# Optimization experiments

Measured on AMD Instinct MI355X. Metric: run time of the kernel, lower is better.

Reference implementation:

```python
import jax, jax.numpy as jnp
import numpy as np

EPS = 1e-6      # zero-token detection eps
LN_EPS = 1e-5   # torch LayerNorm default
H = 8           # num_heads


def setup_inputs() -> dict:
    key = jax.random.key(0)
    ks = jax.random.split(key, 6)
    B, T, D = 4, 2048, 512
    embs = jax.random.normal(ks[0], (B, T, D), jnp.float32)
    labels = jax.random.uniform(ks[1], (B, T), jnp.float32)
    s = 1.0 / np.sqrt(D)
    ln_g = jnp.ones((D,), jnp.float32)
    ln_b = jnp.zeros((D,), jnp.float32)
    in_proj_w = jax.random.uniform(ks[2], (3 * D, D), jnp.float32, -s, s)
    in_proj_b = jnp.zeros((3 * D,), jnp.float32)
    out_w = jax.random.uniform(ks[3], (D, D), jnp.float32, -s, s)
    out_b = jnp.zeros((D,), jnp.float32)
    alpha = jnp.float32(1.0)
    beta = jnp.float32(0.0)
    return {"embs": embs, "labels": labels, "ln_g": ln_g, "ln_b": ln_b,
            "in_proj_w": in_proj_w, "in_proj_b": in_proj_b,
            "out_w": out_w, "out_b": out_b, "alpha": alpha, "beta": beta}


def reference(embs, labels, ln_g, ln_b, in_proj_w, in_proj_b, out_w, out_b, alpha, beta):
    B, T, D = embs.shape
    h, dh = H, D // H
    # pre-LayerNorm
    mu = embs.mean(-1, keepdims=True)
    var = ((embs - mu) ** 2).mean(-1, keepdims=True)
    x = (embs - mu) / jnp.sqrt(var + LN_EPS) * ln_g + ln_b
    # key padding mask from all-zero tokens (computed on normalized x, as in source)
    kpm = jnp.abs(x).sum(-1) <= EPS                      # [B,T] bool
    w = jnp.where(kpm, jnp.float32(0.0), labels)         # zero labels on masked tokens
    # fused qkv projection (nn.MultiheadAttention in_proj)
    qkv = x @ in_proj_w.T + in_proj_b                    # [B,T,3D]
    q, k, v = jnp.split(qkv, 3, axis=-1)
    def sp(a):
        return a.reshape(B, T, h, dh).transpose(0, 2, 1, 3)  # [B,h,T,dh]
    q, k, v = sp(q), sp(k), sp(v)
    scores = jnp.einsum('bhqd,bhkd->bhqk', q, k) / np.sqrt(dh)
    # additive label bias: alpha * labels (broadcast over heads & queries) + beta
    scores = scores + (alpha * w[:, None, None, :] + beta)
    # key padding mask -> -inf (use large negative for stability)
    scores = jnp.where(kpm[:, None, None, :], jnp.float32(-1e30), scores)
    a = jax.nn.softmax(scores, axis=-1)
    o = jnp.einsum('bhqk,bhkd->bhqd', a, v).transpose(0, 2, 1, 3).reshape(B, T, D)
    o = o @ out_w.T + out_b
    o = jnp.nan_to_num(o, nan=0.0, posinf=0.0, neginf=0.0)
    # masked mean pool over T
    m = (~kpm)[..., None].astype(o.dtype)                # [B,T,1]
    pooled = (o * m).sum(1) / jnp.maximum(m.sum(1), 1.0)  # [B,D]
    return pooled
```

## Files before the change

kernel.cpp:

```cpp
#include <hip/hip_runtime.h>
#include <math.h>

#define T 2048
#define D 512
#define NH 8
#define DH 64
#define NB 4
#define NTOK (NB * T)
#define LOG2E 1.44269504f
#define QSCALE (0.125f * LOG2E)

using bf16x8 = __attribute__((ext_vector_type(8))) short;
using f32x4  = __attribute__((ext_vector_type(4))) float;

static __device__ __forceinline__ unsigned short f2bf(float f) {
    union { float f; unsigned u; } v; v.f = f;
    unsigned r = v.u + 0x7fffu + ((v.u >> 16) & 1u);
    return (unsigned short)(r >> 16);
}
#if __has_builtin(__builtin_amdgcn_cvt_pk_bf16_f32)
static __device__ __forceinline__ unsigned pack_bf16_pair(float a, float b) {
    auto r = __builtin_amdgcn_cvt_pk_bf16_f32(a, b);
    union { decltype(r) v; unsigned u; } c; c.v = r;
    return c.u;
}
#else
static __device__ __forceinline__ unsigned pack_bf16_pair(float a, float b) {
    union { float f; unsigned u; } ua, ub; ua.f = a; ub.f = b;
    unsigned ra = ua.u + 0x7fffu + ((ua.u >> 16) & 1u);
    unsigned rb = ub.u + 0x7fffu + ((ub.u >> 16) & 1u);
    return __builtin_amdgcn_perm(rb, ra, 0x07060302);
}
#endif


__global__ __launch_bounds__(256) void ln_kernel(
    const float* __restrict__ embs, const float* __restrict__ labels,
    const float* __restrict__ g, const float* __restrict__ bb,
    const float* __restrict__ alpha_p, const float* __restrict__ beta_p,
    unsigned short* __restrict__ xfrag, float* __restrict__ wexp,
    float* __restrict__ kpmf)
{
    __shared__ __align__(16) unsigned short Xs[16][520];
    int tid = threadIdx.x, wave = tid >> 6, lane = tid & 63;
    int quad = lane >> 4, lm = lane & 15;
    int t16 = blockIdx.x;

    float4 g0 = *(const float4*)(g + lane * 8), g1 = *(const float4*)(g + lane * 8 + 4);
    float4 c0 = *(const float4*)(bb + lane * 8), c1 = *(const float4*)(bb + lane * 8 + 4);
    float gv[8] = {g0.x, g0.y, g0.z, g0.w, g1.x, g1.y, g1.z, g1.w};
    float cv[8] = {c0.x, c0.y, c0.z, c0.w, c1.x, c1.y, c1.z, c1.w};

    for (int tt = 0; tt < 4; ++tt) {
        int n = t16 * 16 + wave * 4 + tt;
        const float* e = embs + (size_t)n * D + lane * 8;
        float4 a4 = *(const float4*)e, b4 = *(const float4*)(e + 4);
        float v[8] = {a4.x, a4.y, a4.z, a4.w, b4.x, b4.y, b4.z, b4.w};

        float s = 0.f, ss = 0.f;
        #pragma unroll
        for (int j = 0; j < 8; ++j) { s += v[j]; ss += v[j] * v[j]; }
        #pragma unroll
        for (int o = 1; o <= 32; o <<= 1) {
            s += __shfl_xor(s, o, 64);
            ss += __shfl_xor(ss, o, 64);
        }
        float mu = s * (1.0f / D);
        float var = ss * (1.0f / D) - mu * mu;
        float rstd = rsqrtf(var + 1e-5f);

        float x[8], as = 0.f;
        #pragma unroll
        for (int j = 0; j < 8; ++j) {
            x[j] = (v[j] - mu) * rstd * gv[j] + cv[j];
            as += fabsf(x[j]);
        }
        uint4 pk;
        pk.x = pack_bf16_pair(x[0], x[1]);
        pk.y = pack_bf16_pair(x[2], x[3]);
        pk.z = pack_bf16_pair(x[4], x[5]);
        pk.w = pack_bf16_pair(x[6], x[7]);
        *(uint4*)&Xs[wave * 4 + tt][lane * 8] = pk;

        #pragma unroll
        for (int o = 1; o <= 32; o <<= 1) as += __shfl_xor(as, o, 64);
        if (lane == 0) {
            int kpm = (as <= 1e-6f);
            kpmf[n] = kpm ? 1.0f : 0.0f;
            wexp[n] = kpm ? 0.0f : __expf(alpha_p[0] * labels[n] + beta_p[0]);
        }
    }
    __syncthreads();
    #pragma unroll
    for (int i = 0; i < 4; ++i) {
        int kc = wave * 4 + i;
        bf16x8 fr = *(const bf16x8*)&Xs[lm][kc * 32 + quad * 8];
        *(bf16x8*)(xfrag + ((size_t)(t16 * 16 + kc) * 64 + lane) * 8) = fr;
    }
}

__global__ __launch_bounds__(256) void wconv_kernel(
    const float* __restrict__ w, unsigned short* __restrict__ wbfrag)
{
    __shared__ __align__(16) unsigned short Ws[16][520];
    int tid = threadIdx.x, wave = tid >> 6, lane = tid & 63;
    int quad = lane >> 4, lm = lane & 15;
    int j16 = blockIdx.x;

    for (int tt = 0; tt < 4; ++tt) {
        int j = j16 * 16 + wave * 4 + tt;
        const float* wp = w + (size_t)j * D + lane * 8;
        float4 a4 = *(const float4*)wp, b4 = *(const float4*)(wp + 4);
        uint4 pk;
        pk.x = pack_bf16_pair(a4.x, a4.y);
        pk.y = pack_bf16_pair(a4.z, a4.w);
        pk.z = pack_bf16_pair(b4.x, b4.y);
        pk.w = pack_bf16_pair(b4.z, b4.w);
        *(uint4*)&Ws[wave * 4 + tt][lane * 8] = pk;
    }
    __syncthreads();
    #pragma unroll
    for (int i = 0; i < 4; ++i) {
        int kc = wave * 4 + i;
        bf16x8 fr = *(const bf16x8*)&Ws[lm][kc * 32 + quad * 8];
        *(bf16x8*)(wbfrag + ((size_t)(j16 * 16 + kc) * 64 + lane) * 8) = fr;
    }
}

__global__ __launch_bounds__(256) void wfrag_fill(
    const float* __restrict__ wexp, unsigned short* __restrict__ vfrag)
{
    int idx = blockIdx.x * 256 + threadIdx.x;
    int lane = idx & 63, chunk = idx >> 6;
    int kk = chunk & 1, t64 = (chunk >> 1) & 31, bh = chunk >> 6;
    int lm = lane & 15, quad = lane >> 4;
    int b_ = bh >> 3;
    size_t base = (((size_t)chunk * 5 + 4) * 64 + lane) * 8;
    if (lm == 0) {
        int key0 = t64 * 64 + kk * 32 + quad * 8;
        const float* wp = wexp + b_ * T + key0;
        unsigned short vv[8];
        #pragma unroll
        for (int e = 0; e < 8; ++e) vv[e] = f2bf(wp[e]);
        *(uint4*)(vfrag + base) = *(uint4*)vv;
    } else {
        uint4 z = {0u, 0u, 0u, 0u};
        *(uint4*)(vfrag + base) = z;
    }
}

__global__ __launch_bounds__(256) void qkv_mfma(
    const unsigned short* __restrict__ xfrag, const unsigned short* __restrict__ wbfrag,
    const float* __restrict__ bias, const float* __restrict__ wexp,
    unsigned short* __restrict__ qfrag, unsigned short* __restrict__ kfrag,
    unsigned short* __restrict__ vfrag)
{
    __shared__ __align__(16) unsigned short Ls[4][64][72];
    int tid = threadIdx.x;
    int wave = tid >> 6, lane = tid & 63, quad = lane >> 4, lm = lane & 15;
    int wr = wave >> 1, wc = wave & 1;
    int m0 = blockIdx.x * 128 + wr * 64;
    int j0 = blockIdx.y * 128 + wc * 64;
    int mt16 = m0 >> 4, jt16 = j0 >> 4;

    f32x4 acc[4][4];
    #pragma unroll
    for (int a = 0; a < 4; ++a)
        #pragma unroll
        for (int b = 0; b < 4; ++b) acc[a][b] = (f32x4){0.f,0.f,0.f,0.f};

    bf16x8 af0[4], bf0[4], af1[4], bf1[4];
    auto load_ab = [&](int kc, bf16x8 (&af)[4], bf16x8 (&bf)[4]) {
        #pragma unroll
        for (int mf = 0; mf < 4; ++mf)
            af[mf] = *(const bf16x8*)(xfrag + ((size_t)((mt16 + mf) * 16 + kc) * 64 + lane) * 8);
        #pragma unroll
        for (int nt = 0; nt < 4; ++nt)
            bf[nt] = *(const bf16x8*)(wbfrag + ((size_t)((jt16 + nt) * 16 + kc) * 64 + lane) * 8);
    };
    auto do_mfma = [&](bf16x8 (&af)[4], bf16x8 (&bf)[4]) {
        #pragma unroll
        for (int mf = 0; mf < 4; ++mf)
            #pragma unroll
            for (int nt = 0; nt < 4; ++nt)
                acc[mf][nt] = __builtin_amdgcn_mfma_f32_16x16x32_bf16(af[mf], bf[nt], acc[mf][nt], 0, 0, 0);
    };

    load_ab(0, af0, bf0);
    for (int kc = 0; kc < 16; kc += 2) {
        load_ab(kc + 1, af1, bf1);
        do_mfma(af0, bf0);
        load_ab((kc + 2) & 15, af0, bf0);
        do_mfma(af1, bf1);
    }

    int part = j0 >> 9;
    int h = (j0 & 511) >> 6;
    int b_ = m0 >> 11, tloc = m0 & (T - 1);
    int bh = b_ * NH + h;
    float bcol[4];
    #pragma unroll
    for (int nt = 0; nt < 4; ++nt) bcol[nt] = bias[j0 + nt * 16 + lm];

    if (part == 2) {
        float wv[4][4];
        #pragma unroll
        for (int mf = 0; mf < 4; ++mf)
            #pragma unroll
            for (int r = 0; r < 4; ++r)
                wv[mf][r] = wexp[b_ * T + tloc + mf * 16 + quad * 4 + r];
        #pragma unroll
        for (int mf = 0; mf < 4; ++mf)
            #pragma unroll
            for (int nt = 0; nt < 4; ++nt) {
                uint2 pw;
                pw.x = pack_bf16_pair((acc[mf][nt][0] + bcol[nt]) * wv[mf][0],
                                      (acc[mf][nt][1] + bcol[nt]) * wv[mf][1]);
                pw.y = pack_bf16_pair((acc[mf][nt][2] + bcol[nt]) * wv[mf][2],
                                      (acc[mf][nt][3] + bcol[nt]) * wv[mf][3]);
                *(uint2*)&Ls[wave][nt * 16 + lm][mf * 16 + quad * 4] = pw;
            }
        #pragma unroll
        for (int nt = 0; nt < 4; ++nt)
            #pragma unroll
            for (int kk = 0; kk < 2; ++kk) {
                bf16x8 fr = *(const bf16x8*)&Ls[wave][nt * 16 + lm][kk * 32 + quad * 8];
                size_t chunk = ((((size_t)bh * 32 + (tloc >> 6)) * 2 + kk) * 5) + nt;
                *(bf16x8*)(vfrag + chunk * 512 + lane * 8) = fr;
            }
    } else {
        float scale = (part == 0) ? QSCALE : 1.0f;
        #pragma unroll
        for (int mf = 0; mf < 4; ++mf)
            #pragma unroll
            for (int nt = 0; nt < 4; ++nt)
                #pragma unroll
                for (int r = 0; r < 4; ++r)
                    Ls[wave][mf * 16 + quad * 4 + r][nt * 16 + lm] =
                        f2bf((acc[mf][nt][r] + bcol[nt]) * scale);
        if (part == 0) {
            #pragma unroll
            for (int mf = 0; mf < 4; ++mf)
                #pragma unroll
                for (int kk = 0; kk < 2; ++kk) {
                    bf16x8 fr = *(const bf16x8*)&Ls[wave][mf * 16 + lm][kk * 32 + quad * 8];
                    size_t chunk = ((size_t)bh * 128 + (tloc >> 4) + mf) * 2 + kk;
                    *(bf16x8*)(qfrag + chunk * 512 + lane * 8) = fr;
                }
        } else {
            #pragma unroll
            for (int nta = 0; nta < 4; ++nta)
                #pragma unroll
                for (int kk = 0; kk < 2; ++kk) {
                    bf16x8 fr = *(const bf16x8*)&Ls[wave][lm * 4 + nta][kk * 32 + quad * 8];
                    size_t chunk = ((((size_t)bh * 32 + (tloc >> 6)) * 2 + kk) * 4) + nta;
                    *(bf16x8*)(kfrag + chunk * 512 + lane * 8) = fr;
                }
        }
    }
}

__global__ __launch_bounds__(256, 2) void attn_mfma(
    const unsigned short* __restrict__ qfrag, const unsigned short* __restrict__ kfrag,
    const unsigned short* __restrict__ vfrag, const float* __restrict__ kpmf,
    float* __restrict__ S)
{
    __shared__ __align__(16) unsigned short Ps[4][64][72];
    __shared__ float Lx[2][2][64];
    int g = blockIdx.x;
    int bh = g & 31, q0 = (g >> 5) * 128;
    int tid = threadIdx.x, wave = tid >> 6, lane = tid & 63;
    int quad = lane >> 4, lm = lane & 15;
    int qh = wave >> 1, ks = wave & 1;
    int qbase = q0 + qh * 64;
    int b_ = bh >> 3, h = bh & 7;

    bf16x8 qf[4][2];
    int t16b = (qbase >> 4);
    #pragma unroll
    for (int mf = 0; mf < 4; ++mf)
        #pragma unroll
        for (int kk = 0; kk < 2; ++kk)
            qf[mf][kk] = *(const bf16x8*)(qfrag +
                (((size_t)(bh * 128 + t16b + mf) * 2 + kk) * 64 + lane) * 8);

    f32x4 accO[4][4], accL[4];
    #pragma unroll
    for (int mf = 0; mf < 4; ++mf) {
        #pragma unroll
        for (int nt = 0; nt < 4; ++nt) accO[mf][nt] = (f32x4){0.f,0.f,0.f,0.f};
        accL[mf] = (f32x4){0.f,0.f,0.f,0.f};
    }

    const unsigned short* kb = kfrag + (size_t)bh * 32 * 8 * 512 + (size_t)lane * 8;
    const unsigned short* vb = vfrag + (size_t)bh * 32 * 10 * 512 + (size_t)lane * 8;
    int t0k = ks * 16;

    bf16x8 kf0[4][2], kf1[4][2];
    auto load_k = [&](int t64, bf16x8 (&kf)[4][2]) {
        const unsigned short* p = kb + (size_t)t64 * 8 * 512;
        #pragma unroll
        for (int kk = 0; kk < 2; ++kk)
            #pragma unroll
            for (int nt = 0; nt < 4; ++nt)
                kf[nt][kk] = *(const bf16x8*)(p + ((size_t)kk * 4 + nt) * 512);
    };

    auto process = [&](int t64, bf16x8 (&kf)[4][2]) {
        const unsigned short* p = vb + (size_t)t64 * 10 * 512;
        bf16x8 vf[5][2];
        #pragma unroll
        for (int kk = 0; kk < 2; ++kk)
            #pragma unroll
            for (int nt = 0; nt < 5; ++nt)
                vf[nt][kk] = *(const bf16x8*)(p + ((size_t)kk * 5 + nt) * 512);

        #pragma unroll
        for (int mf = 0; mf < 4; ++mf) {
            f32x4 s[4];
            #pragma unroll
            for (int nt = 0; nt < 4; ++nt) {
                f32x4 t0 = (f32x4){0.f,0.f,0.f,0.f};
                t0 = __builtin_amdgcn_mfma_f32_16x16x32_bf16(qf[mf][0], kf[nt][0], t0, 0, 0, 0);
                t0 = __builtin_amdgcn_mfma_f32_16x16x32_bf16(qf[mf][1], kf[nt][1], t0, 0, 0, 0);
                s[nt] = t0;
            }
            int rowb = mf * 16 + quad * 4;
            #pragma unroll
            for (int r = 0; r < 4; ++r) {
                float p0 = __builtin_amdgcn_exp2f(s[0][r]);
                float p1 = __builtin_amdgcn_exp2f(s[1][r]);
                float p2 = __builtin_amdgcn_exp2f(s[2][r]);
                float p3 = __builtin_amdgcn_exp2f(s[3][r]);
                uint2 pw;
                pw.x = pack_bf16_pair(p0, p1);
                pw.y = pack_bf16_pair(p2, p3);
                *(uint2*)&Ps[wave][rowb + r][lm * 4] = pw;
            }
        }

        bf16x8 pf[4][2];
        #pragma unroll
        for (int mf = 0; mf < 4; ++mf)
            #pragma unroll
            for (int kk = 0; kk < 2; ++kk)
                pf[mf][kk] = *(const bf16x8*)&Ps[wave][mf * 16 + lm][kk * 32 + quad * 8];

        #pragma unroll
        for (int mf = 0; mf < 4; ++mf) {
            #pragma unroll
            for (int nt = 0; nt < 4; ++nt) {
                accO[mf][nt] = __builtin_amdgcn_mfma_f32_16x16x32_bf16(pf[mf][0], vf[nt][0], accO[mf][nt], 0, 0, 0);
                accO[mf][nt] = __builtin_amdgcn_mfma_f32_16x16x32_bf16(pf[mf][1], vf[nt][1], accO[mf][nt], 0, 0, 0);
            }
            accL[mf] = __builtin_amdgcn_mfma_f32_16x16x32_bf16(pf[mf][0], vf[4][0], accL[mf], 0, 0, 0);
            accL[mf] = __builtin_amdgcn_mfma_f32_16x16x32_bf16(pf[mf][1], vf[4][1], accL[mf], 0, 0, 0);
        }
    };

    load_k(t0k, kf0);
    for (int i = 0; i < 16; i += 2) {
        load_k(t0k + i + 1, kf1);
        process(t0k + i, kf0);
        load_k(t0k + ((i + 2) & 15), kf0);
        process(t0k + i + 1, kf1);
    }

    if (lm == 0) {
        #pragma unroll
        for (int mf = 0; mf < 4; ++mf)
            #pragma unroll
            for (int r = 0; r < 4; ++r)
                Lx[qh][ks][mf * 16 + quad * 4 + r] = accL[mf][r];
    }
    __syncthreads();

    float pooled[4] = {0.f, 0.f, 0.f, 0.f};
    #pragma unroll
    for (int mf = 0; mf < 4; ++mf)
        #pragma unroll
        for (int r = 0; r < 4; ++r) {
            int rloc = mf * 16 + quad * 4 + r;
            float l = Lx[qh][0][rloc] + Lx[qh][1][rloc];
            float w = (1.0f - kpmf[b_ * T + qbase + rloc]) / l;
            #pragma unroll
            for (int nt = 0; nt < 4; ++nt) pooled[nt] += accO[mf][nt][r] * w;
        }
    #pragma unroll
    for (int nt = 0; nt < 4; ++nt) {
        pooled[nt] += __shfl_xor(pooled[nt], 16, 64);
        pooled[nt] += __shfl_xor(pooled[nt], 32, 64);
    }
    if (quad == 0) {
        #pragma unroll
        for (int nt = 0; nt < 4; ++nt)
            atomicAdd(&S[b_ * D + h * DH + nt * 16 + lm], pooled[nt]);
    }
}

__global__ __launch_bounds__(256) void out_kernel(
    const float* __restrict__ S, const float* __restrict__ kpmf,
    const float* __restrict__ Wo, const float* __restrict__ bo,
    float* __restrict__ out)
{
    __shared__ float Sl[512];
    __shared__ float cs[4];
    __shared__ float pr[4][64];
    int b_ = blockIdx.x >> 3;
    int cg = blockIdx.x & 7;
    int tid = threadIdx.x;
    int col = tid & 63, kq = tid >> 6;
    Sl[tid] = S[b_ * D + tid];
    Sl[tid + 256] = S[b_ * D + tid + 256];
    const float* kp = kpmf + b_ * T;
    float c = 0.f;
    for (int t = tid; t < T; t += 256) c += kp[t];
    #pragma unroll
    for (int o = 32; o; o >>= 1) c += __shfl_xor(c, o, 64);
    if ((tid & 63) == 0) cs[tid >> 6] = c;
    __syncthreads();
    float masked = cs[0] + cs[1] + cs[2] + cs[3];
    float cnt = (float)T - masked;
    float inv = 1.0f / fmaxf(cnt, 1.0f);

    int d = cg * 64 + col;
    const float4* wr4 = (const float4*)(Wo + (size_t)d * D + kq * 128);
    float dot = 0.f;
    #pragma unroll 8
    for (int i = 0; i < 32; ++i) {
        float4 w4 = wr4[i];
        int kbase = kq * 128 + i * 4;
        dot += Sl[kbase + 0] * w4.x + Sl[kbase + 1] * w4.y +
               Sl[kbase + 2] * w4.z + Sl[kbase + 3] * w4.w;
    }
    pr[kq][col] = dot;
    __syncthreads();
    if (kq == 0) {
        float tot = pr[0][col] + pr[1][col] + pr[2][col] + pr[3][col];
        out[b_ * D + d] = (tot + bo[d] * cnt) * inv;
    }
}

extern "C" void kernel_launch(void* const* d_in, const int* in_sizes, int n_in,
                              void* d_out, int out_size, void* d_ws, size_t ws_size,
                              hipStream_t stream) {
    const float* embs   = (const float*)d_in[0];
    const float* labels = (const float*)d_in[1];
    const float* ln_g   = (const float*)d_in[2];
    const float* ln_b   = (const float*)d_in[3];
    const float* ipw    = (const float*)d_in[4];
    const float* ipb    = (const float*)d_in[5];
    const float* ow     = (const float*)d_in[6];
    const float* obb    = (const float*)d_in[7];
    const float* alpha  = (const float*)d_in[8];
    const float* beta   = (const float*)d_in[9];
    float* out = (float*)d_out;

    unsigned short* xfrag  = (unsigned short*)d_ws;
    unsigned short* wbfrag = xfrag + (size_t)NTOK * D;
    unsigned short* qfrag  = wbfrag + (size_t)3 * D * D;
    unsigned short* kfrag  = qfrag + (size_t)NTOK * D;
    unsigned short* vfrag  = kfrag + (size_t)NTOK * D;
    float* wexp = (float*)(vfrag + (size_t)32 * 32 * 2 * 5 * 512);
    float* kpmf = wexp + NTOK;
    float* S    = kpmf + NTOK;

    hipMemsetAsync(S, 0, (size_t)NB * D * sizeof(float), stream);
    ln_kernel<<<NTOK / 16, 256, 0, stream>>>(embs, labels, ln_g, ln_b, alpha, beta,
                                             xfrag, wexp, kpmf);
    wconv_kernel<<<(3 * D) / 16, 256, 0, stream>>>(ipw, wbfrag);
    wfrag_fill<<<512, 256, 0, stream>>>(wexp, vfrag);
    dim3 gq(NTOK / 128, (3 * D) / 128);
    qkv_mfma<<<gq, 256, 0, stream>>>(xfrag, wbfrag, ipb, wexp, qfrag, kfrag, vfrag);
    attn_mfma<<<32 * (T / 128), 256, 0, stream>>>(qfrag, kfrag, vfrag, kpmf, S);
    out_kernel<<<NB * 8, 256, 0, stream>>>(S, kpmf, ow, obb, out);
}
```

Baseline: 165.7 us.

## Merge prep kernels, fold weight-row fill into QKV, split attention keys four ways

The LayerNorm and weight-conversion kernels become one launch that picks its role by block index. The separate wfrag_fill kernel is removed, and its work (writing the exp-label weight row into the V fragments) moves into the V-epilogue of the QKV GEMM. The attention kernel now uses 512 threads with four key-split waves per query half instead of two, which halves each wave's key loop and adds a four-way partial-sum reduction. The aim is to cut launch overhead and raise attention parallelism, at the cost of more LDS per block and a changed occupancy target.

```diff
diff --git a/kernel.cpp b/kernel.cpp
--- a/kernel.cpp
+++ b/kernel.cpp
@@ -34,118 +34,91 @@
 #endif
 
 
-__global__ __launch_bounds__(256) void ln_kernel(
+__global__ __launch_bounds__(256) void prep_kernel(
     const float* __restrict__ embs, const float* __restrict__ labels,
     const float* __restrict__ g, const float* __restrict__ bb,
     const float* __restrict__ alpha_p, const float* __restrict__ beta_p,
-    unsigned short* __restrict__ xfrag, float* __restrict__ wexp,
-    float* __restrict__ kpmf)
+    const float* __restrict__ w,
+    unsigned short* __restrict__ xfrag, unsigned short* __restrict__ wbfrag,
+    float* __restrict__ wexp, float* __restrict__ kpmf)
 {
     __shared__ __align__(16) unsigned short Xs[16][520];
     int tid = threadIdx.x, wave = tid >> 6, lane = tid & 63;
     int quad = lane >> 4, lm = lane & 15;
-    int t16 = blockIdx.x;
-
-    float4 g0 = *(const float4*)(g + lane * 8), g1 = *(const float4*)(g + lane * 8 + 4);
-    float4 c0 = *(const float4*)(bb + lane * 8), c1 = *(const float4*)(bb + lane * 8 + 4);
-    float gv[8] = {g0.x, g0.y, g0.z, g0.w, g1.x, g1.y, g1.z, g1.w};
-    float cv[8] = {c0.x, c0.y, c0.z, c0.w, c1.x, c1.y, c1.z, c1.w};
-
-    for (int tt = 0; tt < 4; ++tt) {
-        int n = t16 * 16 + wave * 4 + tt;
-        const float* e = embs + (size_t)n * D + lane * 8;
-        float4 a4 = *(const float4*)e, b4 = *(const float4*)(e + 4);
-        float v[8] = {a4.x, a4.y, a4.z, a4.w, b4.x, b4.y, b4.z, b4.w};
-
-        float s = 0.f, ss = 0.f;
-        #pragma unroll
-        for (int j = 0; j < 8; ++j) { s += v[j]; ss += v[j] * v[j]; }
-        #pragma unroll
-        for (int o = 1; o <= 32; o <<= 1) {
-            s += __shfl_xor(s, o, 64);
-            ss += __shfl_xor(ss, o, 64);
-        }
-        float mu = s * (1.0f / D);
-        float var = ss * (1.0f / D) - mu * mu;
-        float rstd = rsqrtf(var + 1e-5f);
-
-        float x[8], as = 0.f;
-        #pragma unroll
-        for (int j = 0; j < 8; ++j) {
-            x[j] = (v[j] - mu) * rstd * gv[j] + cv[j];
-            as += fabsf(x[j]);
-        }
-        uint4 pk;
-        pk.x = pack_bf16_pair(x[0], x[1]);
-        pk.y = pack_bf16_pair(x[2], x[3]);
-        pk.z = pack_bf16_pair(x[4], x[5]);
-        pk.w = pack_bf16_pair(x[6], x[7]);
-        *(uint4*)&Xs[wave * 4 + tt][lane * 8] = pk;
-
-        #pragma unroll
-        for (int o = 1; o <= 32; o <<= 1) as += __shfl_xor(as, o, 64);
-        if (lane == 0) {
-            int kpm = (as <= 1e-6f);
-            kpmf[n] = kpm ? 1.0f : 0.0f;
-            wexp[n] = kpm ? 0.0f : __expf(alpha_p[0] * labels[n] + beta_p[0]);
-        }
-    }
-    __syncthreads();
-    #pragma unroll
-    for (int i = 0; i < 4; ++i) {
-        int kc = wave * 4 + i;
-        bf16x8 fr = *(const bf16x8*)&Xs[lm][kc * 32 + quad * 8];
-        *(bf16x8*)(xfrag + ((size_t)(t16 * 16 + kc) * 64 + lane) * 8) = fr;
-    }
-}
-
-__global__ __launch_bounds__(256) void wconv_kernel(
-    const float* __restrict__ w, unsigned short* __restrict__ wbfrag)
-{
-    __shared__ __align__(16) unsigned short Ws[16][520];
-    int tid = threadIdx.x, wave = tid >> 6, lane = tid & 63;
-    int quad = lane >> 4, lm = lane & 15;
-    int j16 = blockIdx.x;
-
-    for (int tt = 0; tt < 4; ++tt) {
-        int j = j16 * 16 + wave * 4 + tt;
-        const float* wp = w + (size_t)j * D + lane * 8;
-        float4 a4 = *(const float4*)wp, b4 = *(const float4*)(wp + 4);
-        uint4 pk;
-        pk.x = pack_bf16_pair(a4.x, a4.y);
-        pk.y = pack_bf16_pair(a4.z, a4.w);
-        pk.z = pack_bf16_pair(b4.x, b4.y);
-        pk.w = pack_bf16_pair(b4.z, b4.w);
-        *(uint4*)&Ws[wave * 4 + tt][lane * 8] = pk;
-    }
-    __syncthreads();
-    #pragma unroll
-    for (int i = 0; i < 4; ++i) {
-        int kc = wave * 4 + i;
-        bf16x8 fr = *(const bf16x8*)&Ws[lm][kc * 32 + quad * 8];
-        *(bf16x8*)(wbfrag + ((size_t)(j16 * 16 + kc) * 64 + lane) * 8) = fr;
-    }
-}
-
-__global__ __launch_bounds__(256) void wfrag_fill(
-    const float* __restrict__ wexp, unsigned short* __restrict__ vfrag)
-{
-    int idx = blockIdx.x * 256 + threadIdx.x;
-    int lane = idx & 63, chunk = idx >> 6;
-    int kk = chunk & 1, t64 = (chunk >> 1) & 31, bh = chunk >> 6;
-    int lm = lane & 15, quad = lane >> 4;
-    int b_ = bh >> 3;
-    size_t base = (((size_t)chunk * 5 + 4) * 64 + lane) * 8;
-    if (lm == 0) {
-        int key0 = t64 * 64 + kk * 32 + quad * 8;
-        const float* wp = wexp + b_ * T + key0;
-        unsigned short vv[8];
-        #pragma unroll
-        for (int e = 0; e < 8; ++e) vv[e] = f2bf(wp[e]);
-        *(uint4*)(vfrag + base) = *(uint4*)vv;
+
+    if (blockIdx.x < 512) {
+        int t16 = blockIdx.x;
+        float4 g0 = *(const float4*)(g + lane * 8), g1 = *(const float4*)(g + lane * 8 + 4);
+        float4 c0 = *(const float4*)(bb + lane * 8), c1 = *(const float4*)(bb + lane * 8 + 4);
+        float gv[8] = {g0.x, g0.y, g0.z, g0.w, g1.x, g1.y, g1.z, g1.w};
+        float cv[8] = {c0.x, c0.y, c0.z, c0.w, c1.x, c1.y, c1.z, c1.w};
+
+        for (int tt = 0; tt < 4; ++tt) {
+            int n = t16 * 16 + wave * 4 + tt;
+            const float* e = embs + (size_t)n * D + lane * 8;
+            float4 a4 = *(const float4*)e, b4 = *(const float4*)(e + 4);
+            float v[8] = {a4.x, a4.y, a4.z, a4.w, b4.x, b4.y, b4.z, b4.w};
+
+            float s = 0.f, ss = 0.f;
+            #pragma unroll
+            for (int j = 0; j < 8; ++j) { s += v[j]; ss += v[j] * v[j]; }
+            #pragma unroll
+            for (int o = 1; o <= 32; o <<= 1) {
+                s += __shfl_xor(s, o, 64);
+                ss += __shfl_xor(ss, o, 64);
+            }
+            float mu = s * (1.0f / D);
+            float var = ss * (1.0f / D) - mu * mu;
+            float rstd = rsqrtf(var + 1e-5f);
+
+            float x[8], as = 0.f;
+            #pragma unroll
+            for (int j = 0; j < 8; ++j) {
+                x[j] = (v[j] - mu) * rstd * gv[j] + cv[j];
+                as += fabsf(x[j]);
+            }
+            uint4 pk;
+            pk.x = pack_bf16_pair(x[0], x[1]);
+            pk.y = pack_bf16_pair(x[2], x[3]);
+            pk.z = pack_bf16_pair(x[4], x[5]);
+            pk.w = pack_bf16_pair(x[6], x[7]);
+            *(uint4*)&Xs[wave * 4 + tt][lane * 8] = pk;
+
+            #pragma unroll
+            for (int o = 1; o <= 32; o <<= 1) as += __shfl_xor(as, o, 64);
+            if (lane == 0) {
+                int kpm = (as <= 1e-6f);
+                kpmf[n] = kpm ? 1.0f : 0.0f;
+                wexp[n] = kpm ? 0.0f : __expf(alpha_p[0] * labels[n] + beta_p[0]);
+            }
+        }
+        __syncthreads();
+        #pragma unroll
+        for (int i = 0; i < 4; ++i) {
+            int kc = wave * 4 + i;
+            bf16x8 fr = *(const bf16x8*)&Xs[lm][kc * 32 + quad * 8];
+            *(bf16x8*)(xfrag + ((size_t)(t16 * 16 + kc) * 64 + lane) * 8) = fr;
+        }
     } else {
-        uint4 z = {0u, 0u, 0u, 0u};
-        *(uint4*)(vfrag + base) = z;
+        int j16 = blockIdx.x - 512;
+        for (int tt = 0; tt < 4; ++tt) {
+            int j = j16 * 16 + wave * 4 + tt;
+            const float* wp = w + (size_t)j * D + lane * 8;
+            float4 a4 = *(const float4*)wp, b4 = *(const float4*)(wp + 4);
+            uint4 pk;
+            pk.x = pack_bf16_pair(a4.x, a4.y);
+            pk.y = pack_bf16_pair(a4.z, a4.w);
+            pk.z = pack_bf16_pair(b4.x, b4.y);
+            pk.w = pack_bf16_pair(b4.z, b4.w);
+            *(uint4*)&Xs[wave * 4 + tt][lane * 8] = pk;
+        }
+        __syncthreads();
+        #pragma unroll
+        for (int i = 0; i < 4; ++i) {
+            int kc = wave * 4 + i;
+            bf16x8 fr = *(const bf16x8*)&Xs[lm][kc * 32 + quad * 8];
+            *(bf16x8*)(wbfrag + ((size_t)(j16 * 16 + kc) * 64 + lane) * 8) = fr;
+        }
     }
 }
 
@@ -228,6 +201,26 @@
                 size_t chunk = ((((size_t)bh * 32 + (tloc >> 6)) * 2 + kk) * 5) + nt;
                 *(bf16x8*)(vfrag + chunk * 512 + lane * 8) = fr;
             }
+        {
+            int hsel = wave & 1, tsel = wave >> 1;
+            int hbase = ((blockIdx.y * 128) & 511) >> 6;
+            int t64base = ((blockIdx.x * 128) & (T - 1)) >> 6;
+            int bh2 = b_ * NH + hbase + hsel;
+            int t64a = t64base + tsel;
+            #pragma unroll
+            for (int kk = 0; kk < 2; ++kk) {
+                size_t chunk = ((((size_t)bh2 * 32 + t64a) * 2 + kk) * 5) + 4;
+                uint4 pk = {0u, 0u, 0u, 0u};
+                if (lm == 0) {
+                    const float* wp = wexp + b_ * T + t64a * 64 + kk * 32 + quad * 8;
+                    unsigned short vv[8];
+                    #pragma unroll
+                    for (int e = 0; e < 8; ++e) vv[e] = f2bf(wp[e]);
+                    pk = *(uint4*)vv;
+                }
+                *(uint4*)(vfrag + chunk * 512 + lane * 8) = pk;
+            }
+        }
     } else {
         float scale = (part == 0) ? QSCALE : 1.0f;
         #pragma unroll
@@ -260,18 +253,18 @@
     }
 }
 
-__global__ __launch_bounds__(256, 2) void attn_mfma(
+__global__ __launch_bounds__(512, 4) void attn_mfma(
     const unsigned short* __restrict__ qfrag, const unsigned short* __restrict__ kfrag,
     const unsigned short* __restrict__ vfrag, const float* __restrict__ kpmf,
     float* __restrict__ S)
 {
-    __shared__ __align__(16) unsigned short Ps[4][64][72];
-    __shared__ float Lx[2][2][64];
+    __shared__ __align__(16) unsigned short Ps[8][64][72];
+    __shared__ float Lx[2][4][64];
     int g = blockIdx.x;
     int bh = g & 31, q0 = (g >> 5) * 128;
     int tid = threadIdx.x, wave = tid >> 6, lane = tid & 63;
     int quad = lane >> 4, lm = lane & 15;
-    int qh = wave >> 1, ks = wave & 1;
+    int qh = wave >> 2, ks = wave & 3;
     int qbase = q0 + qh * 64;
     int b_ = bh >> 3, h = bh & 7;
 
@@ -294,7 +287,7 @@
 
     const unsigned short* kb = kfrag + (size_t)bh * 32 * 8 * 512 + (size_t)lane * 8;
     const unsigned short* vb = vfrag + (size_t)bh * 32 * 10 * 512 + (size_t)lane * 8;
-    int t0k = ks * 16;
+    int t0k = ks * 8;
 
     bf16x8 kf0[4][2], kf1[4][2];
     auto load_k = [&](int t64, bf16x8 (&kf)[4][2]) {
@@ -359,10 +352,10 @@
     };
 
     load_k(t0k, kf0);
-    for (int i = 0; i < 16; i += 2) {
+    for (int i = 0; i < 8; i += 2) {
         load_k(t0k + i + 1, kf1);
         process(t0k + i, kf0);
-        load_k(t0k + ((i + 2) & 15), kf0);
+        load_k(t0k + ((i + 2) & 7), kf0);
         process(t0k + i + 1, kf1);
     }
 
@@ -381,7 +374,8 @@
         #pragma unroll
         for (int r = 0; r < 4; ++r) {
             int rloc = mf * 16 + quad * 4 + r;
-            float l = Lx[qh][0][rloc] + Lx[qh][1][rloc];
+            float l = (Lx[qh][0][rloc] + Lx[qh][1][rloc]) +
+                      (Lx[qh][2][rloc] + Lx[qh][3][rloc]);
             float w = (1.0f - kpmf[b_ * T + qbase + rloc]) / l;
             #pragma unroll
             for (int nt = 0; nt < 4; ++nt) pooled[nt] += accO[mf][nt][r] * w;
@@ -466,12 +460,10 @@
     float* S    = kpmf + NTOK;
 
     hipMemsetAsync(S, 0, (size_t)NB * D * sizeof(float), stream);
-    ln_kernel<<<NTOK / 16, 256, 0, stream>>>(embs, labels, ln_g, ln_b, alpha, beta,
-                                             xfrag, wexp, kpmf);
-    wconv_kernel<<<(3 * D) / 16, 256, 0, stream>>>(ipw, wbfrag);
-    wfrag_fill<<<512, 256, 0, stream>>>(wexp, vfrag);
+    prep_kernel<<<512 + 96, 256, 0, stream>>>(embs, labels, ln_g, ln_b, alpha, beta,
+                                              ipw, xfrag, wbfrag, wexp, kpmf);
     dim3 gq(NTOK / 128, (3 * D) / 128);
     qkv_mfma<<<gq, 256, 0, stream>>>(xfrag, wbfrag, ipb, wexp, qfrag, kfrag, vfrag);
-    attn_mfma<<<32 * (T / 128), 256, 0, stream>>>(qfrag, kfrag, vfrag, kpmf, S);
+    attn_mfma<<<32 * (T / 128), 512, 0, stream>>>(qfrag, kfrag, vfrag, kpmf, S);
     out_kernel<<<NB * 8, 256, 0, stream>>>(S, kpmf, ow, obb, out);
 }
```

New measurement: 342.4 us. +106.7%, slower.
